# Performance work log

Measured on AMD Instinct MI355X. Metric: run time of the kernel, lower is better.

## Reference

```python
import jax, jax.numpy as jnp
import numpy as np

C = 256
CI = C // 2  # inter_channel = 128
B, H, W = 8, 64, 64


def setup_inputs() -> dict:
    key = jax.random.key(0)
    ks = jax.random.split(key, 9)
    s = 0.02
    return {
        "x": jax.random.normal(ks[0], (B, C, H, W), jnp.float32),
        "w_phi": jax.random.normal(ks[1], (CI, C), jnp.float32) * s,
        "b_phi": jax.random.normal(ks[2], (CI,), jnp.float32) * s,
        "w_theta": jax.random.normal(ks[3], (CI, C), jnp.float32) * s,
        "b_theta": jax.random.normal(ks[4], (CI,), jnp.float32) * s,
        "w_g": jax.random.normal(ks[5], (CI, C), jnp.float32) * s,
        "b_g": jax.random.normal(ks[6], (CI,), jnp.float32) * s,
        "w_mask": jax.random.normal(ks[7], (C, CI), jnp.float32) * s,
        "b_mask": jax.random.normal(ks[8], (C,), jnp.float32) * s,
    }


def reference(x, w_phi, b_phi, w_theta, b_theta, w_g, b_g, w_mask, b_mask):
    b, c, h, w = x.shape
    n = h * w
    xf = x.reshape(b, c, n)  # [b, c, n]
    # 1x1 convs == per-position channel projections
    phi = jnp.einsum('dc,bcn->bdn', w_phi, xf) + b_phi[:, None]      # [b, ci, n]
    theta = jnp.einsum('dc,bcn->bnd', w_theta, xf) + b_theta[None, None, :]  # [b, n, ci]
    g = jnp.einsum('dc,bcn->bnd', w_g, xf) + b_g[None, None, :]      # [b, n, ci]
    # full self-attention over spatial positions (no scaling, as in source)
    scores = jnp.einsum('bnd,bdm->bnm', theta, phi)                  # [b, n, n]
    attn = jax.nn.softmax(scores, axis=-1)
    y = jnp.einsum('bnm,bmd->bnd', attn, g)                          # [b, n, ci]
    # mask conv (1x1) back to channel dim + residual
    mask = jnp.einsum('cd,bnd->bcn', w_mask, y) + b_mask[:, None]    # [b, c, n]
    return mask.reshape(b, c, h, w) + x
```

## Files before the change

### kernel.cpp

```cpp
#include <hip/hip_runtime.h>

#define BB 8
#define CC 256
#define DD 128
#define NN 4096

#define LOG2E 1.44269504f
#define MSHIFT 32.0f

typedef __attribute__((ext_vector_type(8))) short short8;
typedef __attribute__((ext_vector_type(4))) short short4v;
typedef __attribute__((ext_vector_type(4))) float f32x4;
typedef __attribute__((ext_vector_type(16))) float f32x16;
typedef __attribute__((ext_vector_type(4))) unsigned int u32x4;

static __device__ __forceinline__ unsigned short f2bf(float f) {
    unsigned u = __builtin_bit_cast(unsigned, f);
    u += 0x7FFFu + ((u >> 16) & 1u);
    return (unsigned short)(u >> 16);
}
static __device__ __forceinline__ float bf2f(unsigned short h) {
    unsigned u = ((unsigned)h) << 16;
    return __builtin_bit_cast(float, u);
}
static __device__ __forceinline__ short8 pack8(float4 a, float4 b) {
    short8 r;
    r[0] = (short)f2bf(a.x); r[1] = (short)f2bf(a.y);
    r[2] = (short)f2bf(a.z); r[3] = (short)f2bf(a.w);
    r[4] = (short)f2bf(b.x); r[5] = (short)f2bf(b.y);
    r[6] = (short)f2bf(b.z); r[7] = (short)f2bf(b.w);
    return r;
}
static __device__ __forceinline__ unsigned cvtpk_bf16(float lo, float hi) {
    unsigned r;
    asm("v_cvt_pk_bf16_f32 %0, %1, %2" : "=v"(r) : "v"(lo), "v"(hi));
    return r;
}
static __device__ __forceinline__ void pl32swap(unsigned &a, unsigned &b) {
#if __has_builtin(__builtin_amdgcn_permlane32_swap)
    auto r = __builtin_amdgcn_permlane32_swap((int)a, (int)b, false, false);
    a = (unsigned)r[0]; b = (unsigned)r[1];
#else
    asm("v_permlane32_swap_b32 %0, %1" : "+v"(a), "+v"(b));
#endif
}
static __device__ __forceinline__ void gll16(const void* g, void* l) {
    __builtin_amdgcn_global_load_lds(
        (const __attribute__((address_space(1))) unsigned int*)g,
        (__attribute__((address_space(3))) unsigned int*)l, 16, 0, 0);
}
#define VMWAIT(N) asm volatile("s_waitcnt vmcnt(" #N ")" ::: "memory")

__global__ __launch_bounds__(512, 2) void k_proj(
        const float* __restrict__ x,
        const float* __restrict__ w_phi, const float* __restrict__ b_phi,
        const float* __restrict__ w_theta, const float* __restrict__ b_theta,
        const float* __restrict__ w_g, const float* __restrict__ b_g,
        unsigned short* __restrict__ qws, unsigned short* __restrict__ kws,
        unsigned short* __restrict__ vtws) {
    __shared__ __align__(16) unsigned short xs[128][72];
    __shared__ __align__(16) unsigned short rp[128][136];
    int nb = blockIdx.x * 128, b = blockIdx.y;
    int t = threadIdx.x, lane = t & 63, wave = t >> 6;
    int l16 = lane & 15, l4 = lane >> 4;
    int wd = wave & 3, wn = wave >> 2;

    f32x4 a_th[2][4], a_ph[2][4], a_g[2][4];
#pragma unroll
    for (int mf = 0; mf < 2; mf++)
#pragma unroll
        for (int nf = 0; nf < 4; nf++)
#pragma unroll
            for (int e = 0; e < 4; e++) { a_th[mf][nf][e] = 0.f; a_ph[mf][nf][e] = 0.f; a_g[mf][nf][e] = 0.f; }

    const float* xpb = x + (size_t)b * CC * NN;

    for (int kc = 0; kc < 4; kc++) {
        int c0k = kc * 64;
        __syncthreads();
        {
            float4 xv[4];
#pragma unroll
            for (int j = 0; j < 4; j++) {
                int idx = t + 512 * j;
                int cr = idx >> 5, pos = idx & 31;
                xv[j] = *(const float4*)(xpb + (size_t)(c0k + cr) * NN + nb + pos * 4);
            }
#pragma unroll
            for (int j = 0; j < 4; j++) {
                int idx = t + 512 * j;
                int cr = idx >> 5, pos = idx & 31;
                int col = (cr + 8 * (pos >> 2)) & 63;
                xs[pos * 4 + 0][col] = f2bf(xv[j].x);
                xs[pos * 4 + 1][col] = f2bf(xv[j].y);
                xs[pos * 4 + 2][col] = f2bf(xv[j].z);
                xs[pos * 4 + 3][col] = f2bf(xv[j].w);
            }
        }
        __syncthreads();
        short8 af_t[2][2], af_p[2][2], af_g[2][2];
#pragma unroll
        for (int mf = 0; mf < 2; mf++)
#pragma unroll
            for (int ic = 0; ic < 2; ic++) {
                int d = wd * 32 + mf * 16 + l16;
                int co = c0k + ic * 32 + l4 * 8;
                const float* wpt = w_theta + d * CC + co;
                const float* wpp = w_phi   + d * CC + co;
                const float* wpg = w_g     + d * CC + co;
                af_t[mf][ic] = pack8(*(const float4*)wpt, *(const float4*)(wpt + 4));
                af_p[mf][ic] = pack8(*(const float4*)wpp, *(const float4*)(wpp + 4));
                af_g[mf][ic] = pack8(*(const float4*)wpg, *(const float4*)(wpg + 4));
            }
#pragma unroll
        for (int nf = 0; nf < 4; nf++)
#pragma unroll
            for (int ic = 0; ic < 2; ic++) {
                int ncol = (ic * 32 + l4 * 8 + 8 * (wn * 4 + nf)) & 63;
                short8 bfr = *(const short8*)&xs[wn * 64 + nf * 16 + l16][ncol];
                a_th[0][nf] = __builtin_amdgcn_mfma_f32_16x16x32_bf16(af_t[0][ic], bfr, a_th[0][nf], 0, 0, 0);
                a_th[1][nf] = __builtin_amdgcn_mfma_f32_16x16x32_bf16(af_t[1][ic], bfr, a_th[1][nf], 0, 0, 0);
                a_ph[0][nf] = __builtin_amdgcn_mfma_f32_16x16x32_bf16(af_p[0][ic], bfr, a_ph[0][nf], 0, 0, 0);
                a_ph[1][nf] = __builtin_amdgcn_mfma_f32_16x16x32_bf16(af_p[1][ic], bfr, a_ph[1][nf], 0, 0, 0);
                a_g[0][nf]  = __builtin_amdgcn_mfma_f32_16x16x32_bf16(af_g[0][ic], bfr, a_g[0][nf], 0, 0, 0);
                a_g[1][nf]  = __builtin_amdgcn_mfma_f32_16x16x32_bf16(af_g[1][ic], bfr, a_g[1][nf], 0, 0, 0);
            }
    }
    __syncthreads();

#pragma unroll
    for (int mf = 0; mf < 2; mf++) {
        int d0 = wd * 32 + mf * 16 + l4 * 4;
        float bb[4];
#pragma unroll
        for (int r = 0; r < 4; r++) bb[r] = b_theta[d0 + r];
#pragma unroll
        for (int nf = 0; nf < 4; nf++) {
            short4v pk;
#pragma unroll
            for (int r = 0; r < 4; r++) pk[r] = (short)f2bf((a_th[mf][nf][r] + bb[r]) * LOG2E);
            *(short4v*)&rp[wn * 64 + nf * 16 + l16][d0] = pk;
        }
    }
    __syncthreads();
    {
        unsigned short* outp = qws + (size_t)b * NN * DD;
#pragma unroll
        for (int i = 0; i < 4; i++) {
            int idx = t + 512 * i;
            int n = idx >> 4, dd = (idx & 15) * 8;
            *(short8*)(outp + (size_t)(nb + n) * DD + dd) = *(const short8*)&rp[n][dd];
        }
    }
    __syncthreads();

#pragma unroll
    for (int mf = 0; mf < 2; mf++) {
        int d0 = wd * 32 + mf * 16 + l4 * 4;
        float bb[4];
#pragma unroll
        for (int r = 0; r < 4; r++) bb[r] = b_phi[d0 + r];
#pragma unroll
        for (int nf = 0; nf < 4; nf++) {
            short4v pk;
#pragma unroll
            for (int r = 0; r < 4; r++) pk[r] = (short)f2bf(a_ph[mf][nf][r] + bb[r]);
            *(short4v*)&rp[wn * 64 + nf * 16 + l16][d0] = pk;
        }
    }
    __syncthreads();
    {
        unsigned short* outp = kws + (size_t)b * NN * DD;
#pragma unroll
        for (int i = 0; i < 4; i++) {
            int idx = t + 512 * i;
            int n = idx >> 4, dd = (idx & 15) * 8;
            *(short8*)(outp + (size_t)(nb + n) * DD + dd) = *(const short8*)&rp[n][dd];
        }
    }
    __syncthreads();

#pragma unroll
    for (int mf = 0; mf < 2; mf++) {
        int drow = wd * 32 + mf * 16 + l4 * 4;
        float bb[4];
#pragma unroll
        for (int r = 0; r < 4; r++) bb[r] = b_g[drow + r];
#pragma unroll
        for (int nf = 0; nf < 4; nf++)
#pragma unroll
            for (int r = 0; r < 4; r++)
                rp[drow + r][wn * 64 + nf * 16 + l16] = f2bf(a_g[mf][nf][r] + bb[r]);
    }
    __syncthreads();
    {
        unsigned short* outp = vtws + (size_t)b * DD * NN;
#pragma unroll
        for (int i = 0; i < 4; i++) {
            int idx = t + 512 * i;
            int d = idx >> 4, n0s = (idx & 15) * 8;
            *(short8*)(outp + (size_t)d * NN + nb + n0s) = *(const short8*)&rp[d][n0s];
        }
    }
}

#define QKSTEP(SN, KBN, KC) \
    SN = __builtin_amdgcn_mfma_f32_32x32x16_bf16( \
        *(const short8*)((KBN) + kvo[KC]), qreg[KC], SN, 0, 0, 0);

#define PABUILD(PA, Pa, Pb, Pc, Pd, Pe, Pf_, Pg, Ph) {                                \
    unsigned x0 = cvtpk_bf16(Pa, Pb);                                                 \
    unsigned x1 = cvtpk_bf16(Pc, Pd);                                                 \
    unsigned y0 = cvtpk_bf16(Pe, Pf_);                                                \
    unsigned y1 = cvtpk_bf16(Pg, Ph);                                                 \
    pl32swap(x0, y0); pl32swap(x1, y1);                                               \
    PA[0] = x0; PA[1] = x1; PA[2] = y0; PA[3] = y1; }

#define FBODY(IT, SC, SN) {                                                           \
    if ((IT) + 2 < NIT) {                                                             \
        int mb2 = kbase + ((IT) + 2) * 32;                                            \
        char* W = (char*)smem + (((IT) + 2) & 3) * 16384;                             \
        gll16(kp + (size_t)mb2 * DD + koff[0], W + (wave * 2 + 0) * 1024);            \
        gll16(kp + (size_t)mb2 * DD + koff[1], W + (wave * 2 + 1) * 1024);            \
        gll16(vp + mb2 + voff[0], W + 8192 + (wave * 2 + 0) * 1024);                  \
        gll16(vp + mb2 + voff[1], W + 8192 + (wave * 2 + 1) * 1024);                  \
        VMWAIT(4);                                                                    \
    } else {                                                                          \
        VMWAIT(0);                                                                    \
    }                                                                                 \
    __builtin_amdgcn_s_barrier();                                                     \
    asm volatile("" ::: "memory");                                                    \
    char* KbN = (char*)smem + (((IT) + 1) & 3) * 16384;                               \
    char* Vb  = (char*)smem + ((IT) & 3) * 16384 + 8192;                              \
    _Pragma("unroll") for (int e = 0; e < 16; e++) SN[e] = -MSHIFT;                   \
    float p0, p1, p2, p3, p4, p5, p6, p7, p8, p9, p10, p11, p12, p13, p14, p15;       \
    __builtin_amdgcn_s_setprio(1);                                                    \
    p0 = __builtin_exp2f(SC[0]);  lsum0 += p0;                                        \
    p1 = __builtin_exp2f(SC[1]);  lsum1 += p1;                                        \
    p2 = __builtin_exp2f(SC[2]);  lsum0 += p2;                                        \
    p3 = __builtin_exp2f(SC[3]);  lsum1 += p3;                                        \
    QKSTEP(SN, KbN, 0) QKSTEP(SN, KbN, 1)                                             \
    p4 = __builtin_exp2f(SC[4]);  lsum0 += p4;                                        \
    p5 = __builtin_exp2f(SC[5]);  lsum1 += p5;                                        \
    p6 = __builtin_exp2f(SC[6]);  lsum0 += p6;                                        \
    p7 = __builtin_exp2f(SC[7]);  lsum1 += p7;                                        \
    QKSTEP(SN, KbN, 2) QKSTEP(SN, KbN, 3)                                             \
    u32x4 paA; PABUILD(paA, p0, p1, p2, p3, p4, p5, p6, p7)                           \
    p8  = __builtin_exp2f(SC[8]);  lsum0 += p8;                                       \
    p9  = __builtin_exp2f(SC[9]);  lsum1 += p9;                                       \
    p10 = __builtin_exp2f(SC[10]); lsum0 += p10;                                      \
    p11 = __builtin_exp2f(SC[11]); lsum1 += p11;                                      \
    QKSTEP(SN, KbN, 4) QKSTEP(SN, KbN, 5)                                             \
    p12 = __builtin_exp2f(SC[12]); lsum0 += p12;                                      \
    p13 = __builtin_exp2f(SC[13]); lsum1 += p13;                                      \
    p14 = __builtin_exp2f(SC[14]); lsum0 += p14;                                      \
    p15 = __builtin_exp2f(SC[15]); lsum1 += p15;                                      \
    QKSTEP(SN, KbN, 6) QKSTEP(SN, KbN, 7)                                             \
    u32x4 paB; PABUILD(paB, p8, p9, p10, p11, p12, p13, p14, p15)                     \
    o[0] = __builtin_amdgcn_mfma_f32_32x32x16_bf16(                                   \
        __builtin_bit_cast(short8, paA), *(const short8*)(Vb + 0 * 2048 + vvo[0]), o[0], 0, 0, 0); \
    o[1] = __builtin_amdgcn_mfma_f32_32x32x16_bf16(                                   \
        __builtin_bit_cast(short8, paA), *(const short8*)(Vb + 1 * 2048 + vvo[0]), o[1], 0, 0, 0); \
    o[2] = __builtin_amdgcn_mfma_f32_32x32x16_bf16(                                   \
        __builtin_bit_cast(short8, paA), *(const short8*)(Vb + 2 * 2048 + vvo[0]), o[2], 0, 0, 0); \
    o[3] = __builtin_amdgcn_mfma_f32_32x32x16_bf16(                                   \
        __builtin_bit_cast(short8, paA), *(const short8*)(Vb + 3 * 2048 + vvo[0]), o[3], 0, 0, 0); \
    o[0] = __builtin_amdgcn_mfma_f32_32x32x16_bf16(                                   \
        __builtin_bit_cast(short8, paB), *(const short8*)(Vb + 0 * 2048 + vvo[1]), o[0], 0, 0, 0); \
    o[1] = __builtin_amdgcn_mfma_f32_32x32x16_bf16(                                   \
        __builtin_bit_cast(short8, paB), *(const short8*)(Vb + 1 * 2048 + vvo[1]), o[1], 0, 0, 0); \
    o[2] = __builtin_amdgcn_mfma_f32_32x32x16_bf16(                                   \
        __builtin_bit_cast(short8, paB), *(const short8*)(Vb + 2 * 2048 + vvo[1]), o[2], 0, 0, 0); \
    o[3] = __builtin_amdgcn_mfma_f32_32x32x16_bf16(                                   \
        __builtin_bit_cast(short8, paB), *(const short8*)(Vb + 3 * 2048 + vvo[1]), o[3], 0, 0, 0); \
    __builtin_amdgcn_s_setprio(0);                                                    \
}

__global__ __launch_bounds__(256, 2) void k_flash(
        const unsigned short* __restrict__ q, const unsigned short* __restrict__ kk,
        const unsigned short* __restrict__ vt, unsigned short* __restrict__ opart,
        float* __restrict__ lsums) {
    __shared__ __align__(16) unsigned char smem[65536];

    int bid = blockIdx.x;
    int b   = bid & 7;
    int rem = bid >> 3;
    int ks  = rem >> 5;
    int qt  = rem & 31;
    int qb  = qt * 128;

    int t = threadIdx.x, lane = t & 63, wave = t >> 6;
    int l31 = lane & 31, hi = lane >> 5;

    const unsigned short* qp = q  + (size_t)b * NN * DD;
    const unsigned short* kp = kk + (size_t)b * NN * DD;
    const unsigned short* vp = vt + (size_t)b * DD * NN;

    short8 qreg[8];
    {
        int qrow = qb + wave * 32 + l31;
#pragma unroll
        for (int kc = 0; kc < 8; kc++)
            qreg[kc] = *(const short8*)(qp + (size_t)qrow * DD + kc * 16 + hi * 8);
    }

    int koff[2], voff[2];
#pragma unroll
    for (int j = 0; j < 2; j++) {
        int seg = wave * 2 + j;
        int krow = seg * 4 + (lane >> 4);
        koff[j] = krow * DD + (((lane & 15) ^ (krow & 7)) << 3);
        int vrow = seg * 16 + (lane >> 2);
        voff[j] = vrow * NN + (((lane & 3) ^ ((vrow ^ (vrow >> 2)) & 3)) << 3);
    }

    int kvo[8], vvo[2];
    {
        int e = l31 & 7;
#pragma unroll
        for (int kc = 0; kc < 8; kc++)
            kvo[kc] = l31 * 256 + ((((kc << 1) | hi) ^ e) << 4);
        int sw = (l31 ^ (l31 >> 2)) & 3;
#pragma unroll
        for (int c = 0; c < 2; c++)
            vvo[c] = l31 * 64 + ((((c << 1) | hi) ^ sw) << 4);
    }

    f32x16 o[4];
#pragma unroll
    for (int df = 0; df < 4; df++)
#pragma unroll
        for (int e = 0; e < 16; e++) o[df][e] = 0.f;
    float lsum0 = 0.f, lsum1 = 0.f;

    int kbase = ks * (NN / 2);
    const int NIT = (NN / 2) / 32;

#pragma unroll
    for (int pt = 0; pt < 2; pt++) {
        int mb = kbase + pt * 32;
        char* Kb = (char*)smem + pt * 16384;
#pragma unroll
        for (int j = 0; j < 2; j++) {
            int seg = wave * 2 + j;
            gll16(kp + (size_t)mb * DD + koff[j], Kb + seg * 1024);
            gll16(vp + mb + voff[j], Kb + 8192 + seg * 1024);
        }
    }
    VMWAIT(4);
    __builtin_amdgcn_s_barrier();
    asm volatile("" ::: "memory");

    f32x16 s0, s1;
#pragma unroll
    for (int e = 0; e < 16; e++) s0[e] = -MSHIFT;
    {
        char* Kb0 = (char*)smem;
        __builtin_amdgcn_s_setprio(1);
        QKSTEP(s0, Kb0, 0) QKSTEP(s0, Kb0, 1) QKSTEP(s0, Kb0, 2) QKSTEP(s0, Kb0, 3)
        QKSTEP(s0, Kb0, 4) QKSTEP(s0, Kb0, 5) QKSTEP(s0, Kb0, 6) QKSTEP(s0, Kb0, 7)
        __builtin_amdgcn_s_setprio(0);
    }

    for (int it = 0; it < NIT; it += 2) {
        FBODY(it, s0, s1)
        FBODY(it + 1, s1, s0)
    }

    {
        float lsum = lsum0 + lsum1;
        float tot = lsum + __shfl_xor(lsum, 32);
        if (lane < 32)
            lsums[((size_t)ks * BB + b) * NN + qb + wave * 32 + l31] = tot;
    }
    __syncthreads();
    unsigned short (*Ox)[136] = (unsigned short (*)[136])smem;
#pragma unroll
    for (int df = 0; df < 4; df++)
#pragma unroll
        for (int r = 0; r < 16; r++) {
            int qr = (r & 3) + 8 * (r >> 2) + 4 * hi;
            Ox[wave * 32 + qr][df * 32 + l31] = f2bf(o[df][r]);
        }
    __syncthreads();
    unsigned short* op = opart + (((size_t)ks * BB + b) * NN + qb) * DD;
#pragma unroll
    for (int i = 0; i < 8; i++) {
        int idx = t + 256 * i;
        int nr = idx >> 4, c0 = (idx & 15) * 8;
        *(short8*)(op + (size_t)nr * DD + c0) = *(const short8*)&Ox[nr][c0];
    }
}

__global__ __launch_bounds__(256) void k_maskout(
        const unsigned short* __restrict__ opart, const float* __restrict__ lsums,
        const float* __restrict__ w_mask, const float* __restrict__ b_mask,
        const float* __restrict__ x, float* __restrict__ out) {
    __shared__ __align__(16) unsigned char pool[52480];
    unsigned short (*Ys)[136] = (unsigned short (*)[136])pool;
    float (*Os)[68] = (float (*)[68])(pool + 17408);
    float* invl = (float*)(pool + 52224);
    int nb = blockIdx.x * 64, b = blockIdx.y;
    int t = threadIdx.x, lane = t & 63, wave = t >> 6;
    int l16 = lane & 15, l4 = lane >> 4;

    const unsigned short* o0 = opart + ((size_t)b * NN + nb) * DD;
    const unsigned short* o1 = opart + (((size_t)BB + b) * NN + nb) * DD;
    if (t < 64) {
        float ls0 = lsums[(size_t)b * NN + nb + t];
        float ls1 = lsums[((size_t)BB + b) * NN + nb + t];
        invl[t] = 1.0f / (ls0 + ls1);
    }
    __syncthreads();
#pragma unroll
    for (int i = 0; i < 4; i++) {
        int idx = t + 256 * i;
        int nr = idx >> 4, d0 = (idx & 15) * 8;
        short8 a = *(const short8*)(o0 + (size_t)nr * DD + d0);
        short8 c = *(const short8*)(o1 + (size_t)nr * DD + d0);
        float inv = invl[nr];
        short8 yv;
#pragma unroll
        for (int j = 0; j < 8; j++)
            yv[j] = (short)f2bf((bf2f((unsigned short)a[j]) + bf2f((unsigned short)c[j])) * inv);
        *(short8*)&Ys[nr][d0] = yv;
    }
    __syncthreads();

    for (int cs = 0; cs < 2; cs++) {
        f32x4 acc[2][4];
#pragma unroll
        for (int mf = 0; mf < 2; mf++)
#pragma unroll
            for (int nf = 0; nf < 4; nf++)
#pragma unroll
                for (int e = 0; e < 4; e++) acc[mf][nf][e] = 0.f;

#pragma unroll
        for (int kc = 0; kc < 4; kc++) {
            int d0 = kc * 32 + l4 * 8;
            short8 af[2];
#pragma unroll
            for (int mf = 0; mf < 2; mf++) {
                int c = cs * 128 + wave * 32 + mf * 16 + l16;
                const float* wp = w_mask + c * DD + d0;
                af[mf] = pack8(*(const float4*)wp, *(const float4*)(wp + 4));
            }
#pragma unroll
            for (int nf = 0; nf < 4; nf++) {
                short8 bfr = *(const short8*)&Ys[nf * 16 + l16][d0];
#pragma unroll
                for (int mf = 0; mf < 2; mf++)
                    acc[mf][nf] = __builtin_amdgcn_mfma_f32_16x16x32_bf16(af[mf], bfr, acc[mf][nf], 0, 0, 0);
            }
        }
        __syncthreads();

#pragma unroll
        for (int mf = 0; mf < 2; mf++) {
            int c0 = wave * 32 + mf * 16 + l4 * 4;
            float bb[4];
#pragma unroll
            for (int r = 0; r < 4; r++) bb[r] = b_mask[cs * 128 + c0 + r];
#pragma unroll
            for (int r = 0; r < 4; r++)
#pragma unroll
                for (int nf = 0; nf < 4; nf++)
                    Os[c0 + r][nf * 16 + l16] = acc[mf][nf][r] + bb[r];
        }
        __syncthreads();

        const float* xp = x + (size_t)b * CC * NN + (size_t)cs * 128 * NN + nb;
        float* op = out + (size_t)b * CC * NN + (size_t)cs * 128 * NN + nb;
#pragma unroll
        for (int i = 0; i < 8; i++) {
            int idx = t + 256 * i;
            int c = idx >> 4, nq = (idx & 15) * 4;
            float4 osv = *(const float4*)&Os[c][nq];
            float4 xv = *(const float4*)(xp + (size_t)c * NN + nq);
            float4 ov;
            ov.x = osv.x + xv.x; ov.y = osv.y + xv.y;
            ov.z = osv.z + xv.z; ov.w = osv.w + xv.w;
            *(float4*)(op + (size_t)c * NN + nq) = ov;
        }
    }
}

extern "C" void kernel_launch(void* const* d_in, const int* in_sizes, int n_in,
                              void* d_out, int out_size, void* d_ws, size_t ws_size,
                              hipStream_t stream) {
    const float* x       = (const float*)d_in[0];
    const float* w_phi   = (const float*)d_in[1];
    const float* b_phi   = (const float*)d_in[2];
    const float* w_theta = (const float*)d_in[3];
    const float* b_theta = (const float*)d_in[4];
    const float* w_g     = (const float*)d_in[5];
    const float* b_g     = (const float*)d_in[6];
    const float* w_mask  = (const float*)d_in[7];
    const float* b_mask  = (const float*)d_in[8];
    float* out = (float*)d_out;

    char* ws = (char*)d_ws;
    unsigned short* opart = (unsigned short*)(ws);
    unsigned short* qw    = (unsigned short*)(ws + ((size_t)16 << 20));
    unsigned short* kw    = (unsigned short*)(ws + ((size_t)24 << 20));
    unsigned short* vtw   = (unsigned short*)(ws + ((size_t)32 << 20));
    float*          lsums = (float*)(ws + ((size_t)40 << 20));

    k_proj<<<dim3(NN / 128, BB), 512, 0, stream>>>(x, w_phi, b_phi, w_theta, b_theta,
                                                   w_g, b_g, qw, kw, vtw);
    k_flash<<<dim3(512, 1, 1), 256, 0, stream>>>(qw, kw, vtw, opart, lsums);
    k_maskout<<<dim3(NN / 64, BB), 256, 0, stream>>>(opart, lsums, w_mask, b_mask, x, out);
}
```

Measured before the change: 222.7 us.

## Shrink projection tiles with register prefetch and split mask-out over channel halves

The projection kernel now uses 256-thread blocks over 32 positions instead of 512 threads over 128, giving a 4x larger grid. It prefetches the next x channel chunk into registers while the current chunk is being computed, and reuses a smaller LDS buffer through an aliased view. The mask-out kernel moves its channel-half loop into a grid dimension, so each block handles one half and the Os buffer aliases Ys to cut LDS use. This raises parallelism and occupancy but re-reads weights more often per position and makes each mask-out block recompute the Y normalization.

```diff
diff --git a/kernel.cpp b/kernel.cpp
--- a/kernel.cpp
+++ b/kernel.cpp
@@ -51,154 +51,140 @@
 }
 #define VMWAIT(N) asm volatile("s_waitcnt vmcnt(" #N ")" ::: "memory")
 
-__global__ __launch_bounds__(512, 2) void k_proj(
+__global__ __launch_bounds__(256, 4) void k_proj(
         const float* __restrict__ x,
         const float* __restrict__ w_phi, const float* __restrict__ b_phi,
         const float* __restrict__ w_theta, const float* __restrict__ b_theta,
         const float* __restrict__ w_g, const float* __restrict__ b_g,
         unsigned short* __restrict__ qws, unsigned short* __restrict__ kws,
         unsigned short* __restrict__ vtws) {
-    __shared__ __align__(16) unsigned short xs[128][72];
-    __shared__ __align__(16) unsigned short rp[128][136];
-    int nb = blockIdx.x * 128, b = blockIdx.y;
+    __shared__ __align__(16) unsigned short xs[32][72];
+    __shared__ __align__(16) unsigned short rp[128][40];
+    int nb = blockIdx.x * 32, b = blockIdx.y;
     int t = threadIdx.x, lane = t & 63, wave = t >> 6;
     int l16 = lane & 15, l4 = lane >> 4;
-    int wd = wave & 3, wn = wave >> 2;
-
-    f32x4 a_th[2][4], a_ph[2][4], a_g[2][4];
-#pragma unroll
-    for (int mf = 0; mf < 2; mf++)
-#pragma unroll
-        for (int nf = 0; nf < 4; nf++)
-#pragma unroll
-            for (int e = 0; e < 4; e++) { a_th[mf][nf][e] = 0.f; a_ph[mf][nf][e] = 0.f; a_g[mf][nf][e] = 0.f; }
+
+    f32x4 acc[3][2][2];
+#pragma unroll
+    for (int p = 0; p < 3; p++)
+#pragma unroll
+        for (int mf = 0; mf < 2; mf++)
+#pragma unroll
+            for (int nf = 0; nf < 2; nf++)
+#pragma unroll
+                for (int e = 0; e < 4; e++) acc[p][mf][nf][e] = 0.f;
 
     const float* xpb = x + (size_t)b * CC * NN;
+    int cr = t >> 2;
+    int ng = t & 3;
+    int wcol = (cr + 8 * (ng >> 1)) & 63;
+
+    float4 xv0, xv1;
+    {
+        const float* src = xpb + (size_t)cr * NN + nb + ng * 8;
+        xv0 = *(const float4*)src; xv1 = *(const float4*)(src + 4);
+    }
 
     for (int kc = 0; kc < 4; kc++) {
-        int c0k = kc * 64;
         __syncthreads();
         {
-            float4 xv[4];
-#pragma unroll
-            for (int j = 0; j < 4; j++) {
-                int idx = t + 512 * j;
-                int cr = idx >> 5, pos = idx & 31;
-                xv[j] = *(const float4*)(xpb + (size_t)(c0k + cr) * NN + nb + pos * 4);
+            int n0 = ng * 8;
+            xs[n0 + 0][wcol] = f2bf(xv0.x);
+            xs[n0 + 1][wcol] = f2bf(xv0.y);
+            xs[n0 + 2][wcol] = f2bf(xv0.z);
+            xs[n0 + 3][wcol] = f2bf(xv0.w);
+            xs[n0 + 4][wcol] = f2bf(xv1.x);
+            xs[n0 + 5][wcol] = f2bf(xv1.y);
+            xs[n0 + 6][wcol] = f2bf(xv1.z);
+            xs[n0 + 7][wcol] = f2bf(xv1.w);
+        }
+        __syncthreads();
+        if (kc < 3) {
+            const float* src = xpb + (size_t)((kc + 1) * 64 + cr) * NN + nb + ng * 8;
+            xv0 = *(const float4*)src; xv1 = *(const float4*)(src + 4);
+        }
+        short8 bfr[2][2];
+#pragma unroll
+        for (int nf = 0; nf < 2; nf++)
+#pragma unroll
+            for (int ic = 0; ic < 2; ic++)
+                bfr[nf][ic] = *(const short8*)&xs[nf * 16 + l16][(ic * 32 + l4 * 8 + 8 * nf) & 63];
+
+        int c0k = kc * 64;
+#pragma unroll
+        for (int p = 0; p < 3; p++) {
+            const float* W = (p == 0) ? w_theta : (p == 1) ? w_phi : w_g;
+            short8 af[2][2];
+#pragma unroll
+            for (int mf = 0; mf < 2; mf++)
+#pragma unroll
+                for (int ic = 0; ic < 2; ic++) {
+                    int d = wave * 32 + mf * 16 + l16;
+                    const float* wp = W + d * CC + c0k + ic * 32 + l4 * 8;
+                    af[mf][ic] = pack8(*(const float4*)wp, *(const float4*)(wp + 4));
+                }
+#pragma unroll
+            for (int nf = 0; nf < 2; nf++)
+#pragma unroll
+                for (int ic = 0; ic < 2; ic++)
+#pragma unroll
+                    for (int mf = 0; mf < 2; mf++)
+                        acc[p][mf][nf] = __builtin_amdgcn_mfma_f32_16x16x32_bf16(
+                            af[mf][ic], bfr[nf][ic], acc[p][mf][nf], 0, 0, 0);
+        }
+    }
+
+    unsigned short (*rq)[136] = (unsigned short (*)[136])rp;
+#pragma unroll
+    for (int pr = 0; pr < 2; pr++) {
+        float scl = (pr == 0) ? LOG2E : 1.0f;
+        const float* bias = (pr == 0) ? b_theta : b_phi;
+#pragma unroll
+        for (int mf = 0; mf < 2; mf++) {
+            int d0 = wave * 32 + mf * 16 + l4 * 4;
+            float bb[4];
+#pragma unroll
+            for (int r = 0; r < 4; r++) bb[r] = bias[d0 + r];
+#pragma unroll
+            for (int nf = 0; nf < 2; nf++) {
+                short4v pk;
+#pragma unroll
+                for (int r = 0; r < 4; r++) pk[r] = (short)f2bf((acc[pr][mf][nf][r] + bb[r]) * scl);
+                *(short4v*)&rq[nf * 16 + l16][d0] = pk;
             }
-#pragma unroll
-            for (int j = 0; j < 4; j++) {
-                int idx = t + 512 * j;
-                int cr = idx >> 5, pos = idx & 31;
-                int col = (cr + 8 * (pos >> 2)) & 63;
-                xs[pos * 4 + 0][col] = f2bf(xv[j].x);
-                xs[pos * 4 + 1][col] = f2bf(xv[j].y);
-                xs[pos * 4 + 2][col] = f2bf(xv[j].z);
-                xs[pos * 4 + 3][col] = f2bf(xv[j].w);
+        }
+        __syncthreads();
+        {
+            unsigned short* outp = (pr == 0 ? qws : kws) + (size_t)b * NN * DD;
+#pragma unroll
+            for (int i = 0; i < 2; i++) {
+                int idx = t + 256 * i;
+                int n = idx >> 4, dd = (idx & 15) * 8;
+                *(short8*)(outp + (size_t)(nb + n) * DD + dd) = *(const short8*)&rq[n][dd];
             }
         }
         __syncthreads();
-        short8 af_t[2][2], af_p[2][2], af_g[2][2];
-#pragma unroll
-        for (int mf = 0; mf < 2; mf++)
-#pragma unroll
-            for (int ic = 0; ic < 2; ic++) {
-                int d = wd * 32 + mf * 16 + l16;
-                int co = c0k + ic * 32 + l4 * 8;
-                const float* wpt = w_theta + d * CC + co;
-                const float* wpp = w_phi   + d * CC + co;
-                const float* wpg = w_g     + d * CC + co;
-                af_t[mf][ic] = pack8(*(const float4*)wpt, *(const float4*)(wpt + 4));
-                af_p[mf][ic] = pack8(*(const float4*)wpp, *(const float4*)(wpp + 4));
-                af_g[mf][ic] = pack8(*(const float4*)wpg, *(const float4*)(wpg + 4));
-            }
-#pragma unroll
-        for (int nf = 0; nf < 4; nf++)
-#pragma unroll
-            for (int ic = 0; ic < 2; ic++) {
-                int ncol = (ic * 32 + l4 * 8 + 8 * (wn * 4 + nf)) & 63;
-                short8 bfr = *(const short8*)&xs[wn * 64 + nf * 16 + l16][ncol];
-                a_th[0][nf] = __builtin_amdgcn_mfma_f32_16x16x32_bf16(af_t[0][ic], bfr, a_th[0][nf], 0, 0, 0);
-                a_th[1][nf] = __builtin_amdgcn_mfma_f32_16x16x32_bf16(af_t[1][ic], bfr, a_th[1][nf], 0, 0, 0);
-                a_ph[0][nf] = __builtin_amdgcn_mfma_f32_16x16x32_bf16(af_p[0][ic], bfr, a_ph[0][nf], 0, 0, 0);
-                a_ph[1][nf] = __builtin_amdgcn_mfma_f32_16x16x32_bf16(af_p[1][ic], bfr, a_ph[1][nf], 0, 0, 0);
-                a_g[0][nf]  = __builtin_amdgcn_mfma_f32_16x16x32_bf16(af_g[0][ic], bfr, a_g[0][nf], 0, 0, 0);
-                a_g[1][nf]  = __builtin_amdgcn_mfma_f32_16x16x32_bf16(af_g[1][ic], bfr, a_g[1][nf], 0, 0, 0);
-            }
-    }
-    __syncthreads();
+    }
 
 #pragma unroll
     for (int mf = 0; mf < 2; mf++) {
-        int d0 = wd * 32 + mf * 16 + l4 * 4;
+        int drow = wave * 32 + mf * 16 + l4 * 4;
         float bb[4];
 #pragma unroll
-        for (int r = 0; r < 4; r++) bb[r] = b_theta[d0 + r];
-#pragma unroll
-        for (int nf = 0; nf < 4; nf++) {
-            short4v pk;
-#pragma unroll
-            for (int r = 0; r < 4; r++) pk[r] = (short)f2bf((a_th[mf][nf][r] + bb[r]) * LOG2E);
-            *(short4v*)&rp[wn * 64 + nf * 16 + l16][d0] = pk;
-        }
-    }
-    __syncthreads();
-    {
-        unsigned short* outp = qws + (size_t)b * NN * DD;
-#pragma unroll
-        for (int i = 0; i < 4; i++) {
-            int idx = t + 512 * i;
-            int n = idx >> 4, dd = (idx & 15) * 8;
-            *(short8*)(outp + (size_t)(nb + n) * DD + dd) = *(const short8*)&rp[n][dd];
-        }
-    }
-    __syncthreads();
-
-#pragma unroll
-    for (int mf = 0; mf < 2; mf++) {
-        int d0 = wd * 32 + mf * 16 + l4 * 4;
-        float bb[4];
-#pragma unroll
-        for (int r = 0; r < 4; r++) bb[r] = b_phi[d0 + r];
-#pragma unroll
-        for (int nf = 0; nf < 4; nf++) {
-            short4v pk;
-#pragma unroll
-            for (int r = 0; r < 4; r++) pk[r] = (short)f2bf(a_ph[mf][nf][r] + bb[r]);
-            *(short4v*)&rp[wn * 64 + nf * 16 + l16][d0] = pk;
-        }
-    }
-    __syncthreads();
-    {
-        unsigned short* outp = kws + (size_t)b * NN * DD;
-#pragma unroll
-        for (int i = 0; i < 4; i++) {
-            int idx = t + 512 * i;
-            int n = idx >> 4, dd = (idx & 15) * 8;
-            *(short8*)(outp + (size_t)(nb + n) * DD + dd) = *(const short8*)&rp[n][dd];
-        }
-    }
-    __syncthreads();
-
-#pragma unroll
-    for (int mf = 0; mf < 2; mf++) {
-        int drow = wd * 32 + mf * 16 + l4 * 4;
-        float bb[4];
-#pragma unroll
         for (int r = 0; r < 4; r++) bb[r] = b_g[drow + r];
 #pragma unroll
-        for (int nf = 0; nf < 4; nf++)
+        for (int nf = 0; nf < 2; nf++)
 #pragma unroll
             for (int r = 0; r < 4; r++)
-                rp[drow + r][wn * 64 + nf * 16 + l16] = f2bf(a_g[mf][nf][r] + bb[r]);
+                rp[drow + r][nf * 16 + l16] = f2bf(acc[2][mf][nf][r] + bb[r]);
     }
     __syncthreads();
     {
         unsigned short* outp = vtws + (size_t)b * DD * NN;
 #pragma unroll
-        for (int i = 0; i < 4; i++) {
-            int idx = t + 512 * i;
-            int d = idx >> 4, n0s = (idx & 15) * 8;
+        for (int i = 0; i < 2; i++) {
+            int idx = t + 256 * i;
+            int d = idx >> 2, n0s = (idx & 3) * 8;
             *(short8*)(outp + (size_t)d * NN + nb + n0s) = *(const short8*)&rp[d][n0s];
         }
     }
@@ -396,11 +382,11 @@
         const unsigned short* __restrict__ opart, const float* __restrict__ lsums,
         const float* __restrict__ w_mask, const float* __restrict__ b_mask,
         const float* __restrict__ x, float* __restrict__ out) {
-    __shared__ __align__(16) unsigned char pool[52480];
+    __shared__ __align__(16) unsigned char pool[35072];
     unsigned short (*Ys)[136] = (unsigned short (*)[136])pool;
-    float (*Os)[68] = (float (*)[68])(pool + 17408);
-    float* invl = (float*)(pool + 52224);
-    int nb = blockIdx.x * 64, b = blockIdx.y;
+    float (*Os)[68] = (float (*)[68])pool;
+    float* invl = (float*)(pool + 34816);
+    int nb = blockIdx.x * 64, cs = blockIdx.y, b = blockIdx.z;
     int t = threadIdx.x, lane = t & 63, wave = t >> 6;
     int l16 = lane & 15, l4 = lane >> 4;
 
@@ -427,62 +413,60 @@
     }
     __syncthreads();
 
-    for (int cs = 0; cs < 2; cs++) {
-        f32x4 acc[2][4];
-#pragma unroll
-        for (int mf = 0; mf < 2; mf++)
+    f32x4 acc[2][4];
+#pragma unroll
+    for (int mf = 0; mf < 2; mf++)
+#pragma unroll
+        for (int nf = 0; nf < 4; nf++)
+#pragma unroll
+            for (int e = 0; e < 4; e++) acc[mf][nf][e] = 0.f;
+
+#pragma unroll
+    for (int kc = 0; kc < 4; kc++) {
+        int d0 = kc * 32 + l4 * 8;
+        short8 af[2];
+#pragma unroll
+        for (int mf = 0; mf < 2; mf++) {
+            int c = cs * 128 + wave * 32 + mf * 16 + l16;
+            const float* wp = w_mask + c * DD + d0;
+            af[mf] = pack8(*(const float4*)wp, *(const float4*)(wp + 4));
+        }
+#pragma unroll
+        for (int nf = 0; nf < 4; nf++) {
+            short8 bfr = *(const short8*)&Ys[nf * 16 + l16][d0];
+#pragma unroll
+            for (int mf = 0; mf < 2; mf++)
+                acc[mf][nf] = __builtin_amdgcn_mfma_f32_16x16x32_bf16(af[mf], bfr, acc[mf][nf], 0, 0, 0);
+        }
+    }
+    __syncthreads();
+
+#pragma unroll
+    for (int mf = 0; mf < 2; mf++) {
+        int c0 = wave * 32 + mf * 16 + l4 * 4;
+        float bb[4];
+#pragma unroll
+        for (int r = 0; r < 4; r++) bb[r] = b_mask[cs * 128 + c0 + r];
+#pragma unroll
+        for (int r = 0; r < 4; r++)
 #pragma unroll
             for (int nf = 0; nf < 4; nf++)
-#pragma unroll
-                for (int e = 0; e < 4; e++) acc[mf][nf][e] = 0.f;
-
-#pragma unroll
-        for (int kc = 0; kc < 4; kc++) {
-            int d0 = kc * 32 + l4 * 8;
-            short8 af[2];
-#pragma unroll
-            for (int mf = 0; mf < 2; mf++) {
-                int c = cs * 128 + wave * 32 + mf * 16 + l16;
-                const float* wp = w_mask + c * DD + d0;
-                af[mf] = pack8(*(const float4*)wp, *(const float4*)(wp + 4));
-            }
-#pragma unroll
-            for (int nf = 0; nf < 4; nf++) {
-                short8 bfr = *(const short8*)&Ys[nf * 16 + l16][d0];
-#pragma unroll
-                for (int mf = 0; mf < 2; mf++)
-                    acc[mf][nf] = __builtin_amdgcn_mfma_f32_16x16x32_bf16(af[mf], bfr, acc[mf][nf], 0, 0, 0);
-            }
-        }
-        __syncthreads();
-
-#pragma unroll
-        for (int mf = 0; mf < 2; mf++) {
-            int c0 = wave * 32 + mf * 16 + l4 * 4;
-            float bb[4];
-#pragma unroll
-            for (int r = 0; r < 4; r++) bb[r] = b_mask[cs * 128 + c0 + r];
-#pragma unroll
-            for (int r = 0; r < 4; r++)
-#pragma unroll
-                for (int nf = 0; nf < 4; nf++)
-                    Os[c0 + r][nf * 16 + l16] = acc[mf][nf][r] + bb[r];
-        }
-        __syncthreads();
-
-        const float* xp = x + (size_t)b * CC * NN + (size_t)cs * 128 * NN + nb;
-        float* op = out + (size_t)b * CC * NN + (size_t)cs * 128 * NN + nb;
-#pragma unroll
-        for (int i = 0; i < 8; i++) {
-            int idx = t + 256 * i;
-            int c = idx >> 4, nq = (idx & 15) * 4;
-            float4 osv = *(const float4*)&Os[c][nq];
-            float4 xv = *(const float4*)(xp + (size_t)c * NN + nq);
-            float4 ov;
-            ov.x = osv.x + xv.x; ov.y = osv.y + xv.y;
-            ov.z = osv.z + xv.z; ov.w = osv.w + xv.w;
-            *(float4*)(op + (size_t)c * NN + nq) = ov;
-        }
+                Os[c0 + r][nf * 16 + l16] = acc[mf][nf][r] + bb[r];
+    }
+    __syncthreads();
+
+    const float* xp = x + (size_t)b * CC * NN + (size_t)cs * 128 * NN + nb;
+    float* op = out + (size_t)b * CC * NN + (size_t)cs * 128 * NN + nb;
+#pragma unroll
+    for (int i = 0; i < 8; i++) {
+        int idx = t + 256 * i;
+        int c = idx >> 4, nq = (idx & 15) * 4;
+        float4 osv = *(const float4*)&Os[c][nq];
+        float4 xv = *(const float4*)(xp + (size_t)c * NN + nq);
+        float4 ov;
+        ov.x = osv.x + xv.x; ov.y = osv.y + xv.y;
+        ov.z = osv.z + xv.z; ov.w = osv.w + xv.w;
+        *(float4*)(op + (size_t)c * NN + nq) = ov;
     }
 }
 
@@ -507,8 +491,8 @@
     unsigned short* vtw   = (unsigned short*)(ws + ((size_t)32 << 20));
     float*          lsums = (float*)(ws + ((size_t)40 << 20));
 
-    k_proj<<<dim3(NN / 128, BB), 512, 0, stream>>>(x, w_phi, b_phi, w_theta, b_theta,
-                                                   w_g, b_g, qw, kw, vtw);
+    k_proj<<<dim3(NN / 32, BB), 256, 0, stream>>>(x, w_phi, b_phi, w_theta, b_theta,
+                                                  w_g, b_g, qw, kw, vtw);
     k_flash<<<dim3(512, 1, 1), 256, 0, stream>>>(qw, kw, vtw, opart, lsums);
-    k_maskout<<<dim3(NN / 64, BB), 256, 0, stream>>>(opart, lsums, w_mask, b_mask, x, out);
-}
+    k_maskout<<<dim3(NN / 64, 2, BB), 256, 0, stream>>>(opart, lsums, w_mask, b_mask, x, out);
+}
```

Result: slower. 267.3 us (+20.0%).
